# Performance work log

Measured on AMD Instinct MI355X. Metric: run time of the kernel, lower is better.

Reference implementation:

```python
import jax, jax.numpy as jnp
import numpy as np

DIM = 1024
HID = 2048
E = 8      # num_experts
K = 2      # num_experts_per_tok


def setup_inputs() -> dict:
    key = jax.random.key(0)
    ks = jax.random.split(key, 5)
    s_in = 1.0 / np.sqrt(DIM)
    s_hid = 1.0 / np.sqrt(HID)
    x = jax.random.normal(ks[0], (2, 2048, DIM), dtype=jnp.float32)
    Wg = jax.random.uniform(ks[1], (DIM, E), minval=-s_in, maxval=s_in, dtype=jnp.float32)
    W1 = jax.random.uniform(ks[2], (E, DIM, HID), minval=-s_in, maxval=s_in, dtype=jnp.float32)
    W3 = jax.random.uniform(ks[3], (E, DIM, HID), minval=-s_in, maxval=s_in, dtype=jnp.float32)
    W2 = jax.random.uniform(ks[4], (E, HID, DIM), minval=-s_hid, maxval=s_hid, dtype=jnp.float32)
    return {"x": x, "Wg": Wg, "W1": W1, "W3": W3, "W2": W2}


def reference(x, Wg, W1, W3, W2):
    orig_shape = x.shape
    xt = x.reshape(-1, x.shape[-1])            # [T, D]
    T = xt.shape[0]
    scores = xt @ Wg                            # [T, E] (gate_softmax=False)
    ew, ei = jax.lax.top_k(scores, K)           # [T, K]
    ew = jax.nn.softmax(ew, axis=-1)            # softmax over selected experts
    # combine weights: [T, E], zero for unselected experts
    combine = jnp.zeros((T, E), dtype=xt.dtype)
    combine = combine.at[jnp.arange(T)[:, None], ei].add(ew)
    out = jnp.zeros_like(xt)
    for e in range(E):  # fixed small loop over structurally distinct experts
        h = jax.nn.silu(xt @ W1[e]) * (xt @ W3[e])   # [T, HID] SwiGLU
        out = out + combine[:, e:e + 1] * (h @ W2[e])
    return out.reshape(orig_shape)
```

## Files before the change

### kernel.cpp

```cpp
#include <hip/hip_runtime.h>

typedef unsigned short u16;
typedef unsigned int u32;
using bf16x8 = __attribute__((ext_vector_type(8))) __bf16;
using f32x4  = __attribute__((ext_vector_type(4))) float;

#define T_TOK 4096
#define DIMD  1024
#define HIDN  2048
#define NEXP  8

#define OFF_CNT  0
#define OFF_OFFS 64
#define OFF_TOK  1024
#define OFF_WGT  (OFF_TOK + NEXP*T_TOK*4)
#define OFF_XB   (1<<20)
#define SZ_XB    (T_TOK*DIMD*2)
#define OFF_W1T  (OFF_XB + SZ_XB)
#define SZ_W     (NEXP*DIMD*HIDN*2)
#define OFF_W3T  (OFF_W1T + SZ_W)
#define OFF_W2T  (OFF_W3T + SZ_W)
#define OFF_H    (OFF_W2T + SZ_W)

__device__ __forceinline__ u16 f2bf(float f) {
    u32 u = __float_as_uint(f);
    u32 r = (u + 0x7fff + ((u >> 16) & 1)) >> 16;
    return (u16)r;
}

__device__ __forceinline__ void gl2lds16(const void* g, void* l) {
    __builtin_amdgcn_global_load_lds(
        (__attribute__((address_space(1))) void*)(g),
        (__attribute__((address_space(3))) void*)(l),
        16, 0, 0);
}

__device__ __forceinline__ bf16x8 ldfrag(const u16* base, int r, int s, int q) {
    int idx = r * 64 + ((((s << 2) | q) ^ (r & 7)) << 3);
    union { uint4 u; bf16x8 b; } c;
    c.u = *(const uint4*)(base + idx);
    return c.b;
}

__global__ __launch_bounds__(256) void gate_kernel(
    const float* __restrict__ x, const float* __restrict__ wg,
    int* __restrict__ cnt, int* __restrict__ tok, float* __restrict__ wgt)
{
    int t = blockIdx.x * 4 + (threadIdx.x >> 6);
    int lane = threadIdx.x & 63;
    float s[8];
#pragma unroll
    for (int e = 0; e < 8; e++) s[e] = 0.f;
    const float* xr = x + (size_t)t * DIMD;
#pragma unroll
    for (int i = 0; i < 16; i++) {
        int d = i * 64 + lane;
        float xv = xr[d];
        float4 w0 = *(const float4*)(wg + d * 8);
        float4 w1 = *(const float4*)(wg + d * 8 + 4);
        s[0] += xv * w0.x; s[1] += xv * w0.y;
        s[2] += xv * w0.z; s[3] += xv * w0.w;
        s[4] += xv * w1.x; s[5] += xv * w1.y;
        s[6] += xv * w1.z; s[7] += xv * w1.w;
    }
#pragma unroll
    for (int e = 0; e < 8; e++)
        for (int off = 32; off; off >>= 1) s[e] += __shfl_xor(s[e], off, 64);
    if (lane == 0) {
        int e0 = 0; float b0 = s[0];
        for (int e = 1; e < 8; e++) if (s[e] > b0) { b0 = s[e]; e0 = e; }
        int e1 = (e0 == 0) ? 1 : 0; float b1 = s[e1];
        for (int e = 0; e < 8; e++) if (e != e0 && s[e] > b1) { b1 = s[e]; e1 = e; }
        float ex = __expf(b1 - b0);
        float w0 = 1.f / (1.f + ex);
        float w1 = ex / (1.f + ex);
        int p0 = atomicAdd(&cnt[e0], 1);
        tok[e0 * T_TOK + p0] = t; wgt[e0 * T_TOK + p0] = w0;
        int p1 = atomicAdd(&cnt[e1], 1);
        tok[e1 * T_TOK + p1] = t; wgt[e1 * T_TOK + p1] = w1;
    }
}

__global__ void offs_kernel(const int* __restrict__ cnt, int* __restrict__ offs)
{
    if (threadIdx.x == 0) {
        int a = 0;
        for (int e = 0; e < 8; e++) { offs[e] = a; a += cnt[e]; }
        offs[8] = a;
    }
}

__global__ __launch_bounds__(256) void convx_kernel(
    const float* __restrict__ in, u16* __restrict__ out)
{
    int i = (blockIdx.x * 256 + threadIdx.x) * 4;
    float4 v = *(const float4*)(in + i);
    ushort4 o;
    o.x = f2bf(v.x); o.y = f2bf(v.y); o.z = f2bf(v.z); o.w = f2bf(v.w);
    *(ushort4*)(out + i) = o;
}

__global__ __launch_bounds__(256) void transpose_kernel(
    const float* __restrict__ in, u16* __restrict__ out, int K, int N)
{
    __shared__ u16 t[64 * 72];
    int e = blockIdx.z;
    int n0 = blockIdx.x * 64, k0 = blockIdx.y * 64;
    const float* ip = in + (size_t)e * K * N;
    u16* op = out + (size_t)e * K * N;
    int tid = threadIdx.x;
    int r = tid >> 2, c = (tid & 3) * 16;
    const float4* src = (const float4*)(ip + (size_t)(k0 + r) * N + n0 + c);
    float4 v0 = src[0], v1 = src[1], v2 = src[2], v3 = src[3];
    u16* dstl = t + r * 72 + c;
    dstl[0]  = f2bf(v0.x); dstl[1]  = f2bf(v0.y); dstl[2]  = f2bf(v0.z); dstl[3]  = f2bf(v0.w);
    dstl[4]  = f2bf(v1.x); dstl[5]  = f2bf(v1.y); dstl[6]  = f2bf(v1.z); dstl[7]  = f2bf(v1.w);
    dstl[8]  = f2bf(v2.x); dstl[9]  = f2bf(v2.y); dstl[10] = f2bf(v2.z); dstl[11] = f2bf(v2.w);
    dstl[12] = f2bf(v3.x); dstl[13] = f2bf(v3.y); dstl[14] = f2bf(v3.z); dstl[15] = f2bf(v3.w);
    __syncthreads();
    int n = tid >> 2;
    union { u16 s[16]; uint4 q[2]; } u;
#pragma unroll
    for (int i = 0; i < 16; i++) u.s[i] = t[(c + i) * 72 + n];
    uint4* dst = (uint4*)(op + (size_t)(n0 + n) * K + k0 + c);
    dst[0] = u.q[0]; dst[1] = u.q[1];
}

__global__ __launch_bounds__(256, 2) void gemm1_kernel(
    const u16* __restrict__ xb, const u16* __restrict__ w1t, const u16* __restrict__ w3t,
    const int* __restrict__ cnt, const int* __restrict__ offs,
    const int* __restrict__ tok, const float* __restrict__ wgt,
    u16* __restrict__ H)
{
    const int e = blockIdx.z, mt = blockIdx.y, nt = blockIdx.x;
    const int ce = cnt[e];
    if (mt * 128 >= ce) return;
    const int base = offs[e];
    const int* tokp = tok + e * T_TOK;

    __shared__ u16 smem[128 * 64 + 64 * 64 + 64 * 64];
    u16* As  = smem;
    u16* B1s = smem + 128 * 64;
    u16* B2s = B1s + 64 * 64;

    const int tid = threadIdx.x;
    const int lane = tid & 63, q = lane >> 4, ln = lane & 15;
    const int wv = tid >> 6;
    const int wm = (wv & 1) * 64, wn = (wv >> 1) * 32;
    const int wbase = tid & ~63;

    f32x4 acc1[4][2], acc2[4][2];
#pragma unroll
    for (int a = 0; a < 4; a++)
#pragma unroll
        for (int b = 0; b < 2; b++) { acc1[a][b] = {0.f,0.f,0.f,0.f}; acc2[a][b] = {0.f,0.f,0.f,0.f}; }

    const u16* w1p = w1t + ((size_t)e * HIDN + nt * 64) * DIMD;
    const u16* w3p = w3t + ((size_t)e * HIDN + nt * 64) * DIMD;

    for (int k0 = 0; k0 < DIMD; k0 += 64) {
        __syncthreads();
#pragma unroll
        for (int i = 0; i < 4; i++) {
            int slot = i * 256 + tid;
            int m = slot >> 3;
            int bk = (slot & 7) ^ (m & 7);
            int mg = mt * 128 + m;
            int trow = (mg < ce) ? tokp[mg] : 0;
            gl2lds16(xb + (size_t)trow * DIMD + k0 + bk * 8, As + (i * 256 + wbase) * 8);
        }
#pragma unroll
        for (int i = 0; i < 2; i++) {
            int slot = i * 256 + tid;
            int n = slot >> 3;
            int bk = (slot & 7) ^ (n & 7);
            gl2lds16(w1p + (size_t)n * DIMD + k0 + bk * 8, B1s + (i * 256 + wbase) * 8);
            gl2lds16(w3p + (size_t)n * DIMD + k0 + bk * 8, B2s + (i * 256 + wbase) * 8);
        }
        __syncthreads();
#pragma unroll
        for (int s = 0; s < 2; s++) {
            bf16x8 af[4];
#pragma unroll
            for (int mf = 0; mf < 4; mf++) af[mf] = ldfrag(As, wm + mf * 16 + ln, s, q);
#pragma unroll
            for (int nf = 0; nf < 2; nf++) {
                bf16x8 b1 = ldfrag(B1s, wn + nf * 16 + ln, s, q);
                bf16x8 b2 = ldfrag(B2s, wn + nf * 16 + ln, s, q);
#pragma unroll
                for (int mf = 0; mf < 4; mf++) {
                    acc1[mf][nf] = __builtin_amdgcn_mfma_f32_16x16x32_bf16(af[mf], b1, acc1[mf][nf], 0, 0, 0);
                    acc2[mf][nf] = __builtin_amdgcn_mfma_f32_16x16x32_bf16(af[mf], b2, acc2[mf][nf], 0, 0, 0);
                }
            }
        }
    }

    const float* wr = wgt + e * T_TOK;
#pragma unroll
    for (int mf = 0; mf < 4; mf++) {
#pragma unroll
        for (int r = 0; r < 4; r++) {
            int mg = mt * 128 + wm + mf * 16 + q * 4 + r;
            if (mg < ce) {
                float wv_ = wr[mg];
                size_t hrow = (size_t)(base + mg) * HIDN + nt * 64 + wn;
#pragma unroll
                for (int nf = 0; nf < 2; nf++) {
                    float c1 = acc1[mf][nf][r], c2 = acc2[mf][nf][r];
                    float h = (c1 / (1.f + __expf(-c1))) * c2 * wv_;
                    H[hrow + nf * 16 + ln] = f2bf(h);
                }
            }
        }
    }
}

__global__ __launch_bounds__(256, 2) void gemm2_kernel(
    const u16* __restrict__ H, const u16* __restrict__ w2t,
    const int* __restrict__ cnt, const int* __restrict__ offs,
    const int* __restrict__ tok, float* __restrict__ out)
{
    const int e = blockIdx.z, mt = blockIdx.y, nt = blockIdx.x;
    const int ce = cnt[e];
    if (mt * 128 >= ce) return;
    const int base = offs[e];
    const int* tokp = tok + e * T_TOK;

    __shared__ u16 smem[128 * 64 + 128 * 64];
    u16* As = smem;
    u16* Bs = smem + 128 * 64;

    const int tid = threadIdx.x;
    const int lane = tid & 63, q = lane >> 4, ln = lane & 15;
    const int wv = tid >> 6;
    const int wm = (wv & 1) * 64, wn = (wv >> 1) * 64;
    const int wbase = tid & ~63;

    f32x4 av[4][4];
#pragma unroll
    for (int a = 0; a < 4; a++)
#pragma unroll
        for (int b = 0; b < 4; b++) av[a][b] = {0.f,0.f,0.f,0.f};

    const u16* w2p = w2t + ((size_t)e * DIMD + nt * 128) * HIDN;

    for (int k0 = 0; k0 < HIDN; k0 += 64) {
        __syncthreads();
#pragma unroll
        for (int i = 0; i < 4; i++) {
            int slot = i * 256 + tid;
            int m = slot >> 3;
            int bk = (slot & 7) ^ (m & 7);
            int mg = mt * 128 + m;
            int ar = base + ((mg < ce) ? mg : 0);
            gl2lds16(H + (size_t)ar * HIDN + k0 + bk * 8, As + (i * 256 + wbase) * 8);
            gl2lds16(w2p + (size_t)m * HIDN + k0 + bk * 8, Bs + (i * 256 + wbase) * 8);
        }
        __syncthreads();
#pragma unroll
        for (int s = 0; s < 2; s++) {
            bf16x8 af[4], bfr[4];
#pragma unroll
            for (int mf = 0; mf < 4; mf++) af[mf]  = ldfrag(As, wm + mf * 16 + ln, s, q);
#pragma unroll
            for (int nf = 0; nf < 4; nf++) bfr[nf] = ldfrag(Bs, wn + nf * 16 + ln, s, q);
#pragma unroll
            for (int mf = 0; mf < 4; mf++)
#pragma unroll
                for (int nf = 0; nf < 4; nf++)
                    av[mf][nf] = __builtin_amdgcn_mfma_f32_16x16x32_bf16(af[mf], bfr[nf], av[mf][nf], 0, 0, 0);
        }
    }

#pragma unroll
    for (int mf = 0; mf < 4; mf++) {
#pragma unroll
        for (int r = 0; r < 4; r++) {
            int mg = mt * 128 + wm + mf * 16 + q * 4 + r;
            if (mg < ce) {
                int tko = tokp[mg];
                float* orow = out + (size_t)tko * DIMD + nt * 128 + wn;
#pragma unroll
                for (int nf = 0; nf < 4; nf++)
                    atomicAdd(orow + nf * 16 + ln, av[mf][nf][r]);
            }
        }
    }
}

extern "C" void kernel_launch(void* const* d_in, const int* in_sizes, int n_in,
                              void* d_out, int out_size, void* d_ws, size_t ws_size,
                              hipStream_t stream)
{
    const float* x  = (const float*)d_in[0];
    const float* wg = (const float*)d_in[1];
    const float* w1 = (const float*)d_in[2];
    const float* w3 = (const float*)d_in[3];
    const float* w2 = (const float*)d_in[4];

    char* ws = (char*)d_ws;
    int*   cnt  = (int*)(ws + OFF_CNT);
    int*   offs = (int*)(ws + OFF_OFFS);
    int*   tok  = (int*)(ws + OFF_TOK);
    float* wgt  = (float*)(ws + OFF_WGT);
    u16*   xb   = (u16*)(ws + OFF_XB);
    u16*   w1t  = (u16*)(ws + OFF_W1T);
    u16*   w3t  = (u16*)(ws + OFF_W3T);
    u16*   w2t  = (u16*)(ws + OFF_W2T);
    u16*   Hbuf = (u16*)(ws + OFF_H);
    float* outp = (float*)d_out;

    hipMemsetAsync(ws + OFF_CNT, 0, 64, stream);
    hipMemsetAsync(d_out, 0, (size_t)T_TOK * DIMD * 4, stream);

    gate_kernel<<<T_TOK / 4, 256, 0, stream>>>(x, wg, cnt, tok, wgt);
    offs_kernel<<<1, 64, 0, stream>>>(cnt, offs);

    convx_kernel<<<(T_TOK * DIMD) / 1024, 256, 0, stream>>>(x, xb);

    transpose_kernel<<<dim3(HIDN / 64, DIMD / 64, NEXP), 256, 0, stream>>>(w1, w1t, DIMD, HIDN);
    transpose_kernel<<<dim3(HIDN / 64, DIMD / 64, NEXP), 256, 0, stream>>>(w3, w3t, DIMD, HIDN);
    transpose_kernel<<<dim3(DIMD / 64, HIDN / 64, NEXP), 256, 0, stream>>>(w2, w2t, HIDN, DIMD);

    gemm1_kernel<<<dim3(HIDN / 64, T_TOK / 128, NEXP), 256, 0, stream>>>(
        xb, w1t, w3t, cnt, offs, tok, wgt, Hbuf);
    gemm2_kernel<<<dim3(DIMD / 128, T_TOK / 128, NEXP), 256, 0, stream>>>(
        Hbuf, w2t, cnt, offs, tok, outp);
}
```

Before: 552.6 us.

## Fuse x conversion into gate, merge transposes, split-K gemm2, raise occupancy

```diff
diff --git a/kernel.cpp b/kernel.cpp
--- a/kernel.cpp
+++ b/kernel.cpp
@@ -44,7 +44,8 @@
 
 __global__ __launch_bounds__(256) void gate_kernel(
     const float* __restrict__ x, const float* __restrict__ wg,
-    int* __restrict__ cnt, int* __restrict__ tok, float* __restrict__ wgt)
+    int* __restrict__ cnt, int* __restrict__ tok, float* __restrict__ wgt,
+    u16* __restrict__ xb)
 {
     int t = blockIdx.x * 4 + (threadIdx.x >> 6);
     int lane = threadIdx.x & 63;
@@ -52,10 +53,12 @@
 #pragma unroll
     for (int e = 0; e < 8; e++) s[e] = 0.f;
     const float* xr = x + (size_t)t * DIMD;
+    u16* xbr = xb + (size_t)t * DIMD;
 #pragma unroll
     for (int i = 0; i < 16; i++) {
         int d = i * 64 + lane;
         float xv = xr[d];
+        xbr[d] = f2bf(xv);
         float4 w0 = *(const float4*)(wg + d * 8);
         float4 w1 = *(const float4*)(wg + d * 8 + 4);
         s[0] += xv * w0.x; s[1] += xv * w0.y;
@@ -90,17 +93,38 @@
     }
 }
 
-__global__ __launch_bounds__(256) void convx_kernel(
-    const float* __restrict__ in, u16* __restrict__ out)
-{
-    int i = (blockIdx.x * 256 + threadIdx.x) * 4;
-    float4 v = *(const float4*)(in + i);
-    ushort4 o;
-    o.x = f2bf(v.x); o.y = f2bf(v.y); o.z = f2bf(v.z); o.w = f2bf(v.w);
-    *(ushort4*)(out + i) = o;
-}
-
-__global__ __launch_bounds__(256) void transpose_kernel(
+__global__ __launch_bounds__(256) void transpose2_kernel(
+    const float* __restrict__ inA, u16* __restrict__ outA,
+    const float* __restrict__ inB, u16* __restrict__ outB,
+    int K, int N)
+{
+    __shared__ u16 t[64 * 72];
+    int z = blockIdx.z;
+    int e = z & 7;
+    const float* in = (z < 8) ? inA : inB;
+    u16* out = (z < 8) ? outA : outB;
+    int n0 = blockIdx.x * 64, k0 = blockIdx.y * 64;
+    const float* ip = in + (size_t)e * K * N;
+    u16* op = out + (size_t)e * K * N;
+    int tid = threadIdx.x;
+    int r = tid >> 2, c = (tid & 3) * 16;
+    const float4* src = (const float4*)(ip + (size_t)(k0 + r) * N + n0 + c);
+    float4 v0 = src[0], v1 = src[1], v2 = src[2], v3 = src[3];
+    u16* dstl = t + r * 72 + c;
+    dstl[0]  = f2bf(v0.x); dstl[1]  = f2bf(v0.y); dstl[2]  = f2bf(v0.z); dstl[3]  = f2bf(v0.w);
+    dstl[4]  = f2bf(v1.x); dstl[5]  = f2bf(v1.y); dstl[6]  = f2bf(v1.z); dstl[7]  = f2bf(v1.w);
+    dstl[8]  = f2bf(v2.x); dstl[9]  = f2bf(v2.y); dstl[10] = f2bf(v2.z); dstl[11] = f2bf(v2.w);
+    dstl[12] = f2bf(v3.x); dstl[13] = f2bf(v3.y); dstl[14] = f2bf(v3.z); dstl[15] = f2bf(v3.w);
+    __syncthreads();
+    int n = tid >> 2;
+    union { u16 s[16]; uint4 q[2]; } u;
+#pragma unroll
+    for (int i = 0; i < 16; i++) u.s[i] = t[(c + i) * 72 + n];
+    uint4* dst = (uint4*)(op + (size_t)(n0 + n) * K + k0 + c);
+    dst[0] = u.q[0]; dst[1] = u.q[1];
+}
+
+__global__ __launch_bounds__(256) void transpose1_kernel(
     const float* __restrict__ in, u16* __restrict__ out, int K, int N)
 {
     __shared__ u16 t[64 * 72];
@@ -126,7 +150,7 @@
     dst[0] = u.q[0]; dst[1] = u.q[1];
 }
 
-__global__ __launch_bounds__(256, 2) void gemm1_kernel(
+__global__ __launch_bounds__(256, 4) void gemm1_kernel(
     const u16* __restrict__ xb, const u16* __restrict__ w1t, const u16* __restrict__ w3t,
     const int* __restrict__ cnt, const int* __restrict__ offs,
     const int* __restrict__ tok, const float* __restrict__ wgt,
@@ -149,6 +173,17 @@
     const int wm = (wv & 1) * 64, wn = (wv >> 1) * 32;
     const int wbase = tid & ~63;
 
+    const u16* arow[4];
+#pragma unroll
+    for (int i = 0; i < 4; i++) {
+        int slot = i * 256 + tid;
+        int m = slot >> 3;
+        int bk = (slot & 7) ^ (m & 7);
+        int mg = mt * 128 + m;
+        int trow = (mg < ce) ? tokp[mg] : 0;
+        arow[i] = xb + (size_t)trow * DIMD + bk * 8;
+    }
+
     f32x4 acc1[4][2], acc2[4][2];
 #pragma unroll
     for (int a = 0; a < 4; a++)
@@ -161,14 +196,8 @@
     for (int k0 = 0; k0 < DIMD; k0 += 64) {
         __syncthreads();
 #pragma unroll
-        for (int i = 0; i < 4; i++) {
-            int slot = i * 256 + tid;
-            int m = slot >> 3;
-            int bk = (slot & 7) ^ (m & 7);
-            int mg = mt * 128 + m;
-            int trow = (mg < ce) ? tokp[mg] : 0;
-            gl2lds16(xb + (size_t)trow * DIMD + k0 + bk * 8, As + (i * 256 + wbase) * 8);
-        }
+        for (int i = 0; i < 4; i++)
+            gl2lds16(arow[i] + k0, As + (i * 256 + wbase) * 8);
 #pragma unroll
         for (int i = 0; i < 2; i++) {
             int slot = i * 256 + tid;
@@ -216,12 +245,13 @@
     }
 }
 
-__global__ __launch_bounds__(256, 2) void gemm2_kernel(
+__global__ __launch_bounds__(256, 4) void gemm2_kernel(
     const u16* __restrict__ H, const u16* __restrict__ w2t,
     const int* __restrict__ cnt, const int* __restrict__ offs,
     const int* __restrict__ tok, float* __restrict__ out)
 {
-    const int e = blockIdx.z, mt = blockIdx.y, nt = blockIdx.x;
+    const int e = blockIdx.z & 7, kh = blockIdx.z >> 3;
+    const int mt = blockIdx.y, nt = blockIdx.x;
     const int ce = cnt[e];
     if (mt * 128 >= ce) return;
     const int base = offs[e];
@@ -237,25 +267,33 @@
     const int wm = (wv & 1) * 64, wn = (wv >> 1) * 64;
     const int wbase = tid & ~63;
 
+    const u16* arow[4];
+    const u16* brow[4];
+    const u16* w2p = w2t + ((size_t)e * DIMD + nt * 128) * HIDN;
+#pragma unroll
+    for (int i = 0; i < 4; i++) {
+        int slot = i * 256 + tid;
+        int m = slot >> 3;
+        int bk = (slot & 7) ^ (m & 7);
+        int mg = mt * 128 + m;
+        int ar = base + ((mg < ce) ? mg : 0);
+        arow[i] = H + (size_t)ar * HIDN + bk * 8;
+        brow[i] = w2p + (size_t)m * HIDN + bk * 8;
+    }
+
     f32x4 av[4][4];
 #pragma unroll
     for (int a = 0; a < 4; a++)
 #pragma unroll
         for (int b = 0; b < 4; b++) av[a][b] = {0.f,0.f,0.f,0.f};
 
-    const u16* w2p = w2t + ((size_t)e * DIMD + nt * 128) * HIDN;
-
-    for (int k0 = 0; k0 < HIDN; k0 += 64) {
+    const int kbeg = kh * (HIDN / 2), kend = kbeg + HIDN / 2;
+    for (int k0 = kbeg; k0 < kend; k0 += 64) {
         __syncthreads();
 #pragma unroll
         for (int i = 0; i < 4; i++) {
-            int slot = i * 256 + tid;
-            int m = slot >> 3;
-            int bk = (slot & 7) ^ (m & 7);
-            int mg = mt * 128 + m;
-            int ar = base + ((mg < ce) ? mg : 0);
-            gl2lds16(H + (size_t)ar * HIDN + k0 + bk * 8, As + (i * 256 + wbase) * 8);
-            gl2lds16(w2p + (size_t)m * HIDN + k0 + bk * 8, Bs + (i * 256 + wbase) * 8);
+            gl2lds16(arow[i] + k0, As + (i * 256 + wbase) * 8);
+            gl2lds16(brow[i] + k0, Bs + (i * 256 + wbase) * 8);
         }
         __syncthreads();
 #pragma unroll
@@ -314,17 +352,16 @@
     hipMemsetAsync(ws + OFF_CNT, 0, 64, stream);
     hipMemsetAsync(d_out, 0, (size_t)T_TOK * DIMD * 4, stream);
 
-    gate_kernel<<<T_TOK / 4, 256, 0, stream>>>(x, wg, cnt, tok, wgt);
+    gate_kernel<<<T_TOK / 4, 256, 0, stream>>>(x, wg, cnt, tok, wgt, xb);
     offs_kernel<<<1, 64, 0, stream>>>(cnt, offs);
 
-    convx_kernel<<<(T_TOK * DIMD) / 1024, 256, 0, stream>>>(x, xb);
-
-    transpose_kernel<<<dim3(HIDN / 64, DIMD / 64, NEXP), 256, 0, stream>>>(w1, w1t, DIMD, HIDN);
-    transpose_kernel<<<dim3(HIDN / 64, DIMD / 64, NEXP), 256, 0, stream>>>(w3, w3t, DIMD, HIDN);
-    transpose_kernel<<<dim3(DIMD / 64, HIDN / 64, NEXP), 256, 0, stream>>>(w2, w2t, HIDN, DIMD);
+    transpose2_kernel<<<dim3(HIDN / 64, DIMD / 64, 16), 256, 0, stream>>>(
+        w1, w1t, w3, w3t, DIMD, HIDN);
+    transpose1_kernel<<<dim3(DIMD / 64, HIDN / 64, NEXP), 256, 0, stream>>>(
+        w2, w2t, HIDN, DIMD);
 
     gemm1_kernel<<<dim3(HIDN / 64, T_TOK / 128, NEXP), 256, 0, stream>>>(
         xb, w1t, w3t, cnt, offs, tok, wgt, Hbuf);
-    gemm2_kernel<<<dim3(DIMD / 128, T_TOK / 128, NEXP), 256, 0, stream>>>(
+    gemm2_kernel<<<dim3(DIMD / 128, T_TOK / 128, NEXP * 2), 256, 0, stream>>>(
         Hbuf, w2t, cnt, offs, tok, outp);
 }
```

After: 531.7 us. 3.8% less time.

## Fuse prep kernels, load A fragments from global, replace atomics with scatter-reduce

Applied to the files above, without the earlier changes.

```diff
diff --git a/kernel.cpp b/kernel.cpp
--- a/kernel.cpp
+++ b/kernel.cpp
@@ -11,9 +11,10 @@
 #define NEXP  8
 
 #define OFF_CNT  0
-#define OFF_OFFS 64
-#define OFF_TOK  1024
+#define OFF_TCNT 64
+#define OFF_TOK  16448
 #define OFF_WGT  (OFF_TOK + NEXP*T_TOK*4)
+#define OFF_T2S  (OFF_WGT + NEXP*T_TOK*4)
 #define OFF_XB   (1<<20)
 #define SZ_XB    (T_TOK*DIMD*2)
 #define OFF_W1T  (OFF_XB + SZ_XB)
@@ -21,6 +22,7 @@
 #define OFF_W3T  (OFF_W1T + SZ_W)
 #define OFF_W2T  (OFF_W3T + SZ_W)
 #define OFF_H    (OFF_W2T + SZ_W)
+#define OFF_OS   OFF_W1T
 
 __device__ __forceinline__ u16 f2bf(float f) {
     u32 u = __float_as_uint(f);
@@ -42,9 +44,22 @@
     return c.b;
 }
 
+__device__ __forceinline__ bf16x8 ldfragG(const u16* rowp, int k) {
+    union { uint4 u; bf16x8 b; } c;
+    c.u = *(const uint4*)(rowp + k);
+    return c.b;
+}
+
+__device__ __forceinline__ int prefix_cnt(const int* cnt, int e) {
+    int b = 0;
+    for (int j = 0; j < NEXP; j++) b += (j < e) ? cnt[j] : 0;
+    return b;
+}
+
 __global__ __launch_bounds__(256) void gate_kernel(
     const float* __restrict__ x, const float* __restrict__ wg,
-    int* __restrict__ cnt, int* __restrict__ tok, float* __restrict__ wgt)
+    int* __restrict__ cnt, int* __restrict__ tok, float* __restrict__ wgt,
+    u16* __restrict__ xb)
 {
     int t = blockIdx.x * 4 + (threadIdx.x >> 6);
     int lane = threadIdx.x & 63;
@@ -52,10 +67,12 @@
 #pragma unroll
     for (int e = 0; e < 8; e++) s[e] = 0.f;
     const float* xr = x + (size_t)t * DIMD;
+    u16* xbr = xb + (size_t)t * DIMD;
 #pragma unroll
     for (int i = 0; i < 16; i++) {
         int d = i * 64 + lane;
         float xv = xr[d];
+        xbr[d] = f2bf(xv);
         float4 w0 = *(const float4*)(wg + d * 8);
         float4 w1 = *(const float4*)(wg + d * 8 + 4);
         s[0] += xv * w0.x; s[1] += xv * w0.y;
@@ -81,30 +98,37 @@
     }
 }
 
-__global__ void offs_kernel(const int* __restrict__ cnt, int* __restrict__ offs)
-{
-    if (threadIdx.x == 0) {
-        int a = 0;
-        for (int e = 0; e < 8; e++) { offs[e] = a; a += cnt[e]; }
-        offs[8] = a;
-    }
-}
-
-__global__ __launch_bounds__(256) void convx_kernel(
-    const float* __restrict__ in, u16* __restrict__ out)
-{
-    int i = (blockIdx.x * 256 + threadIdx.x) * 4;
-    float4 v = *(const float4*)(in + i);
-    ushort4 o;
-    o.x = f2bf(v.x); o.y = f2bf(v.y); o.z = f2bf(v.z); o.w = f2bf(v.w);
-    *(ushort4*)(out + i) = o;
+__global__ __launch_bounds__(256) void map_kernel(
+    const int* __restrict__ cnt, const int* __restrict__ tok,
+    int* __restrict__ tcnt, int* __restrict__ t2s)
+{
+    int gid = blockIdx.x * 256 + threadIdx.x;
+    int e = gid >> 12, i = gid & 4095;
+    if (i >= cnt[e]) return;
+    int base = prefix_cnt(cnt, e);
+    int t = tok[e * T_TOK + i];
+    int idx = atomicAdd(&tcnt[t], 1);
+    t2s[2 * t + idx] = base + i;
 }
 
 __global__ __launch_bounds__(256) void transpose_kernel(
-    const float* __restrict__ in, u16* __restrict__ out, int K, int N)
+    const float* __restrict__ w1, u16* __restrict__ w1t,
+    const float* __restrict__ w3, u16* __restrict__ w3t,
+    const float* __restrict__ w2, u16* __restrict__ w2t)
 {
     __shared__ u16 t[64 * 72];
-    int e = blockIdx.z;
+    int z = blockIdx.z;
+    int e = z & 7;
+    const float* in; u16* out; int K, N;
+    if (z < 16) {
+        K = DIMD; N = HIDN;
+        in = (z < 8) ? w1 : w3; out = (z < 8) ? w1t : w3t;
+        if ((int)blockIdx.y >= K / 64) return;
+    } else {
+        K = HIDN; N = DIMD;
+        in = w2; out = w2t;
+        if ((int)blockIdx.x >= N / 64) return;
+    }
     int n0 = blockIdx.x * 64, k0 = blockIdx.y * 64;
     const float* ip = in + (size_t)e * K * N;
     u16* op = out + (size_t)e * K * N;
@@ -126,22 +150,20 @@
     dst[0] = u.q[0]; dst[1] = u.q[1];
 }
 
-__global__ __launch_bounds__(256, 2) void gemm1_kernel(
+__global__ __launch_bounds__(256, 4) void gemm1_kernel(
     const u16* __restrict__ xb, const u16* __restrict__ w1t, const u16* __restrict__ w3t,
-    const int* __restrict__ cnt, const int* __restrict__ offs,
-    const int* __restrict__ tok, const float* __restrict__ wgt,
-    u16* __restrict__ H)
+    const int* __restrict__ cnt, const int* __restrict__ tok,
+    const float* __restrict__ wgt, u16* __restrict__ H)
 {
     const int e = blockIdx.z, mt = blockIdx.y, nt = blockIdx.x;
     const int ce = cnt[e];
     if (mt * 128 >= ce) return;
-    const int base = offs[e];
+    const int base = prefix_cnt(cnt, e);
     const int* tokp = tok + e * T_TOK;
 
-    __shared__ u16 smem[128 * 64 + 64 * 64 + 64 * 64];
-    u16* As  = smem;
-    u16* B1s = smem + 128 * 64;
-    u16* B2s = B1s + 64 * 64;
+    __shared__ u16 smem[64 * 64 * 2];
+    u16* B1s = smem;
+    u16* B2s = smem + 64 * 64;
 
     const int tid = threadIdx.x;
     const int lane = tid & 63, q = lane >> 4, ln = lane & 15;
@@ -149,6 +171,14 @@
     const int wm = (wv & 1) * 64, wn = (wv >> 1) * 32;
     const int wbase = tid & ~63;
 
+    const u16* arp[4];
+#pragma unroll
+    for (int mf = 0; mf < 4; mf++) {
+        int mg = mt * 128 + wm + mf * 16 + ln;
+        int tr = (mg < ce) ? tokp[mg] : 0;
+        arp[mf] = xb + (size_t)tr * DIMD;
+    }
+
     f32x4 acc1[4][2], acc2[4][2];
 #pragma unroll
     for (int a = 0; a < 4; a++)
@@ -160,15 +190,6 @@
 
     for (int k0 = 0; k0 < DIMD; k0 += 64) {
         __syncthreads();
-#pragma unroll
-        for (int i = 0; i < 4; i++) {
-            int slot = i * 256 + tid;
-            int m = slot >> 3;
-            int bk = (slot & 7) ^ (m & 7);
-            int mg = mt * 128 + m;
-            int trow = (mg < ce) ? tokp[mg] : 0;
-            gl2lds16(xb + (size_t)trow * DIMD + k0 + bk * 8, As + (i * 256 + wbase) * 8);
-        }
 #pragma unroll
         for (int i = 0; i < 2; i++) {
             int slot = i * 256 + tid;
@@ -182,7 +203,7 @@
         for (int s = 0; s < 2; s++) {
             bf16x8 af[4];
 #pragma unroll
-            for (int mf = 0; mf < 4; mf++) af[mf] = ldfrag(As, wm + mf * 16 + ln, s, q);
+            for (int mf = 0; mf < 4; mf++) af[mf] = ldfragG(arp[mf], k0 + s * 32 + q * 8);
 #pragma unroll
             for (int nf = 0; nf < 2; nf++) {
                 bf16x8 b1 = ldfrag(B1s, wn + nf * 16 + ln, s, q);
@@ -216,20 +237,16 @@
     }
 }
 
-__global__ __launch_bounds__(256, 2) void gemm2_kernel(
+__global__ __launch_bounds__(256, 4) void gemm2_kernel(
     const u16* __restrict__ H, const u16* __restrict__ w2t,
-    const int* __restrict__ cnt, const int* __restrict__ offs,
-    const int* __restrict__ tok, float* __restrict__ out)
+    const int* __restrict__ cnt, float* __restrict__ os)
 {
     const int e = blockIdx.z, mt = blockIdx.y, nt = blockIdx.x;
     const int ce = cnt[e];
     if (mt * 128 >= ce) return;
-    const int base = offs[e];
-    const int* tokp = tok + e * T_TOK;
-
-    __shared__ u16 smem[128 * 64 + 128 * 64];
-    u16* As = smem;
-    u16* Bs = smem + 128 * 64;
+    const int base = prefix_cnt(cnt, e);
+
+    __shared__ u16 Bs[128 * 64];
 
     const int tid = threadIdx.x;
     const int lane = tid & 63, q = lane >> 4, ln = lane & 15;
@@ -237,6 +254,14 @@
     const int wm = (wv & 1) * 64, wn = (wv >> 1) * 64;
     const int wbase = tid & ~63;
 
+    const u16* arp[4];
+#pragma unroll
+    for (int mf = 0; mf < 4; mf++) {
+        int mg = mt * 128 + wm + mf * 16 + ln;
+        int sr = base + ((mg < ce) ? mg : 0);
+        arp[mf] = H + (size_t)sr * HIDN;
+    }
+
     f32x4 av[4][4];
 #pragma unroll
     for (int a = 0; a < 4; a++)
@@ -252,9 +277,6 @@
             int slot = i * 256 + tid;
             int m = slot >> 3;
             int bk = (slot & 7) ^ (m & 7);
-            int mg = mt * 128 + m;
-            int ar = base + ((mg < ce) ? mg : 0);
-            gl2lds16(H + (size_t)ar * HIDN + k0 + bk * 8, As + (i * 256 + wbase) * 8);
             gl2lds16(w2p + (size_t)m * HIDN + k0 + bk * 8, Bs + (i * 256 + wbase) * 8);
         }
         __syncthreads();
@@ -262,7 +284,7 @@
         for (int s = 0; s < 2; s++) {
             bf16x8 af[4], bfr[4];
 #pragma unroll
-            for (int mf = 0; mf < 4; mf++) af[mf]  = ldfrag(As, wm + mf * 16 + ln, s, q);
+            for (int mf = 0; mf < 4; mf++) af[mf]  = ldfragG(arp[mf], k0 + s * 32 + q * 8);
 #pragma unroll
             for (int nf = 0; nf < 4; nf++) bfr[nf] = ldfrag(Bs, wn + nf * 16 + ln, s, q);
 #pragma unroll
@@ -279,14 +301,27 @@
         for (int r = 0; r < 4; r++) {
             int mg = mt * 128 + wm + mf * 16 + q * 4 + r;
             if (mg < ce) {
-                int tko = tokp[mg];
-                float* orow = out + (size_t)tko * DIMD + nt * 128 + wn;
+                float* orow = os + (size_t)(base + mg) * DIMD + nt * 128 + wn;
 #pragma unroll
                 for (int nf = 0; nf < 4; nf++)
-                    atomicAdd(orow + nf * 16 + ln, av[mf][nf][r]);
+                    orow[nf * 16 + ln] = av[mf][nf][r];
             }
         }
     }
+}
+
+__global__ __launch_bounds__(256) void reduce_kernel(
+    const float* __restrict__ os, const int* __restrict__ t2s,
+    float* __restrict__ out)
+{
+    int t = blockIdx.x;
+    int s0 = t2s[2 * t], s1 = t2s[2 * t + 1];
+    int c = threadIdx.x * 4;
+    const float4* a = (const float4*)(os + (size_t)s0 * DIMD + c);
+    const float4* b = (const float4*)(os + (size_t)s1 * DIMD + c);
+    float4 va = *a, vb = *b;
+    float4 o; o.x = va.x + vb.x; o.y = va.y + vb.y; o.z = va.z + vb.z; o.w = va.w + vb.w;
+    *(float4*)(out + (size_t)t * DIMD + c) = o;
 }
 
 extern "C" void kernel_launch(void* const* d_in, const int* in_sizes, int n_in,
@@ -301,30 +336,29 @@
 
     char* ws = (char*)d_ws;
     int*   cnt  = (int*)(ws + OFF_CNT);
-    int*   offs = (int*)(ws + OFF_OFFS);
+    int*   tcnt = (int*)(ws + OFF_TCNT);
     int*   tok  = (int*)(ws + OFF_TOK);
     float* wgt  = (float*)(ws + OFF_WGT);
+    int*   t2s  = (int*)(ws + OFF_T2S);
     u16*   xb   = (u16*)(ws + OFF_XB);
     u16*   w1t  = (u16*)(ws + OFF_W1T);
     u16*   w3t  = (u16*)(ws + OFF_W3T);
     u16*   w2t  = (u16*)(ws + OFF_W2T);
     u16*   Hbuf = (u16*)(ws + OFF_H);
+    float* osb  = (float*)(ws + OFF_OS);
     float* outp = (float*)d_out;
 
-    hipMemsetAsync(ws + OFF_CNT, 0, 64, stream);
-    hipMemsetAsync(d_out, 0, (size_t)T_TOK * DIMD * 4, stream);
-
-    gate_kernel<<<T_TOK / 4, 256, 0, stream>>>(x, wg, cnt, tok, wgt);
-    offs_kernel<<<1, 64, 0, stream>>>(cnt, offs);
-
-    convx_kernel<<<(T_TOK * DIMD) / 1024, 256, 0, stream>>>(x, xb);
-
-    transpose_kernel<<<dim3(HIDN / 64, DIMD / 64, NEXP), 256, 0, stream>>>(w1, w1t, DIMD, HIDN);
-    transpose_kernel<<<dim3(HIDN / 64, DIMD / 64, NEXP), 256, 0, stream>>>(w3, w3t, DIMD, HIDN);
-    transpose_kernel<<<dim3(DIMD / 64, HIDN / 64, NEXP), 256, 0, stream>>>(w2, w2t, HIDN, DIMD);
+    hipMemsetAsync(ws, 0, 64 + T_TOK * 4, stream);
+
+    gate_kernel<<<T_TOK / 4, 256, 0, stream>>>(x, wg, cnt, tok, wgt, xb);
+    map_kernel<<<(NEXP * T_TOK) / 256, 256, 0, stream>>>(cnt, tok, tcnt, t2s);
+
+    transpose_kernel<<<dim3(32, 32, 24), 256, 0, stream>>>(w1, w1t, w3, w3t, w2, w2t);
 
     gemm1_kernel<<<dim3(HIDN / 64, T_TOK / 128, NEXP), 256, 0, stream>>>(
-        xb, w1t, w3t, cnt, offs, tok, wgt, Hbuf);
+        xb, w1t, w3t, cnt, tok, wgt, Hbuf);
     gemm2_kernel<<<dim3(DIMD / 128, T_TOK / 128, NEXP), 256, 0, stream>>>(
-        Hbuf, w2t, cnt, offs, tok, outp);
-}
+        Hbuf, w2t, cnt, osb);
+
+    reduce_kernel<<<T_TOK, 256, 0, stream>>>(osb, t2s, outp);
+}
```

Result: slower. 636.7 us (+15.2%).
